# Optimization experiments

Hardware: AMD Instinct MI355X
Metric: run time of the kernel (lower is better)

The kernel has to match this reference:

```python
import jax, jax.numpy as jnp
import numpy as np

DIM = 192
NH = 4
B, H, W = 4, 128, 128


def _conv1x1(x, w, b):
    # x: [b,c,h,w], w: [o,c], b: [o]
    return jnp.einsum('oc,bchw->bohw', w, x) + b[None, :, None, None]


def _dwconv3(x, w, b):
    # depthwise 3x3, w: [C,1,3,3]
    y = jax.lax.conv_general_dilated(
        x, w, window_strides=(1, 1), padding='SAME',
        feature_group_count=x.shape[1],
        dimension_numbers=('NCHW', 'OIHW', 'NCHW'))
    return y + b[None, :, None, None]


def _to_heads(x, nh):
    b, c, h, w = x.shape
    return x.reshape(b, nh, c // nh, h * w)  # b head c (hw)


def _l2norm(x):
    # torch F.normalize(dim=-1): x / max(||x||, eps)
    n = jnp.sqrt(jnp.sum(x * x, axis=-1, keepdims=True))
    return x / jnp.maximum(n, 1e-12)


def _chan_attn(q, k, v, temp):
    # q,k,v: [b,head,c,n]; temp: [head,1,1] -> broadcasts over [b,head,c,c]
    scores = jnp.einsum('bhcn,bhdn->bhcd', q, k) * temp
    a = jax.nn.softmax(scores, axis=-1)
    return jnp.einsum('bhcd,bhdn->bhcn', a, v)


def setup_inputs() -> dict:
    key = jax.random.key(0)
    ks = jax.random.split(key, 16)
    d3 = 3 * DIM
    inp = {
        'sar': jax.random.normal(ks[0], (B, DIM, H, W), jnp.float32),
        'ms': jax.random.normal(ks[1], (B, DIM, H, W), jnp.float32),
        'ms_qkv_w': jax.random.normal(ks[2], (d3, DIM), jnp.float32) * 0.02,
        'ms_qkv_b': jnp.zeros((d3,), jnp.float32),
        'ms_dw_w': jax.random.normal(ks[3], (d3, 1, 3, 3), jnp.float32) * 0.1,
        'ms_dw_b': jnp.zeros((d3,), jnp.float32),
        'ms_temp': jnp.ones((NH, 1, 1), jnp.float32),
        'sar_qkv_w': jax.random.normal(ks[4], (d3, DIM), jnp.float32) * 0.02,
        'sar_qkv_b': jnp.zeros((d3,), jnp.float32),
        'sar_dw_w': jax.random.normal(ks[5], (d3, 1, 3, 3), jnp.float32) * 0.1,
        'sar_dw_b': jnp.zeros((d3,), jnp.float32),
        'sar_temp': jnp.ones((NH, 1, 1), jnp.float32),
        'ms_proj_w': jax.random.normal(ks[6], (DIM, 2 * DIM), jnp.float32) * 0.02,
        'ms_proj_b': jnp.zeros((DIM,), jnp.float32),
        'sar_proj_w': jax.random.normal(ks[7], (DIM, DIM), jnp.float32) * 0.02,
        'sar_proj_b': jnp.zeros((DIM,), jnp.float32),
    }
    return inp


def reference(sar, ms, ms_qkv_w, ms_qkv_b, ms_dw_w, ms_dw_b, ms_temp,
              sar_qkv_w, sar_qkv_b, sar_dw_w, sar_dw_b, sar_temp,
              ms_proj_w, ms_proj_b, sar_proj_w, sar_proj_b):
    b, c, h, w = ms.shape

    ms_qkv = _dwconv3(_conv1x1(ms, ms_qkv_w, ms_qkv_b), ms_dw_w, ms_dw_b)
    ms_q, ms_k, ms_v = jnp.split(ms_qkv, 3, axis=1)
    ms_q = _l2norm(_to_heads(ms_q, NH))
    ms_k = _l2norm(_to_heads(ms_k, NH))
    ms_v = _to_heads(ms_v, NH)

    sar_qkv = _dwconv3(_conv1x1(sar, sar_qkv_w, sar_qkv_b), sar_dw_w, sar_dw_b)
    sar_q, sar_k, sar_v = jnp.split(sar_qkv, 3, axis=1)
    sar_q = _l2norm(_to_heads(sar_q, NH))
    sar_k = _l2norm(_to_heads(sar_k, NH))
    sar_v = _to_heads(sar_v, NH)

    ms_self = _chan_attn(ms_q, ms_k, ms_v, ms_temp).reshape(b, c, h, w)
    sar_self = _chan_attn(sar_q, sar_k, sar_v, sar_temp).reshape(b, c, h, w)
    cross = _chan_attn(sar_q, ms_k, sar_v, ms_temp).reshape(b, c, h, w)

    sar_out = sar + _conv1x1(sar_self, sar_proj_w, sar_proj_b)
    ms_cat = jnp.concatenate([ms_self, cross + ms_self], axis=1)
    ms_out = ms + _conv1x1(ms_cat, ms_proj_w, ms_proj_b)
    return (sar_out, ms_out)
```

## Files before the change

### kernel.cpp

```cpp
#include <hip/hip_runtime.h>
#include <hip/hip_bf16.h>
#include <cstdint>

#define DIMC 192
#define BB 4
#define NN 16384
#define D3 576
#define CHD 48
#define WWID 128
#define HHGT 128
#define NCK 64
#define CKW 256

typedef short short8 __attribute__((ext_vector_type(8)));
typedef float f32x4 __attribute__((ext_vector_type(4)));

union FragU { uint4 u4; short8 s8; };

__device__ __forceinline__ float bf2f(uint16_t v) {
    return __uint_as_float(((uint32_t)v) << 16);
}
__device__ __forceinline__ float2 upk2(uint32_t u) {
    float2 r;
    r.x = __uint_as_float(u << 16);
    r.y = __uint_as_float(u & 0xffff0000u);
    return r;
}
__device__ __forceinline__ uint16_t f2bf(float f) {
    uint32_t x = __float_as_uint(f);
    return (uint16_t)((x + 0x7fffu + ((x >> 16) & 1u)) >> 16);
}
__device__ __forceinline__ uint4 pack8(const uint16_t* v) {
    uint4 u;
    u.x = (uint32_t)v[0] | ((uint32_t)v[1] << 16);
    u.y = (uint32_t)v[2] | ((uint32_t)v[3] << 16);
    u.z = (uint32_t)v[4] | ((uint32_t)v[5] << 16);
    u.w = (uint32_t)v[6] | ((uint32_t)v[7] << 16);
    return u;
}

__global__ __launch_bounds__(256) void k_prep(
    const float* __restrict__ w0, const float* __restrict__ w1,
    const float* __restrict__ w2, const float* __restrict__ w3,
    uint16_t* __restrict__ o0, uint16_t* __restrict__ o1,
    uint16_t* __restrict__ o2a, uint16_t* __restrict__ o2b,
    uint16_t* __restrict__ o3)
{
    int i = blockIdx.x * 256 + threadIdx.x;
    if (i < 110592) { o0[i] = f2bf(w0[i]); return; }
    i -= 110592;
    if (i < 110592) { o1[i] = f2bf(w1[i]); return; }
    i -= 110592;
    if (i < 36864) {
        const int o = i / DIMC, c = i % DIMC;
        o2a[i] = f2bf(w2[o * 384 + c] + w2[o * 384 + DIMC + c]);
        o2b[i] = f2bf(w2[o * 384 + DIMC + c]);
        return;
    }
    i -= 36864;
    if (i < 36864) o3[i] = f2bf(w3[i]);
}

__global__ __launch_bounds__(256, 2) void k_conv_both(
    const float* __restrict__ ms, const float* __restrict__ sarp,
    const uint16_t* __restrict__ w_ms, const uint16_t* __restrict__ w_sar,
    const float* __restrict__ b_ms, const float* __restrict__ b_sar,
    uint16_t* __restrict__ out_ms, uint16_t* __restrict__ out_sar)
{
    __shared__ uint16_t xs[128][200];
    __shared__ uint16_t wstA[64][200];
    const int t = threadIdx.x;
    const int bid = blockIdx.x;
    const int path = bid >> 9;
    const int rem = bid & 511;
    const int nb = rem & 127, b = rem >> 7;
    const int n0 = nb * 128;

    const float* x        = path ? sarp  : ms;
    const uint16_t* wsrc  = path ? w_sar : w_ms;
    const float* bias     = path ? b_sar : b_ms;
    uint16_t* out         = path ? out_sar : out_ms;

    const int lane = t & 63, wvid = t >> 6;
    const int lm = lane & 15, g = lane >> 4;
    const int wm = wvid >> 1, wn = wvid & 1;
    const int wm_ = t >> 2, wq = t & 3;

    {
        const int sn = t & 127, kh = t >> 7;
        const float* xcol = x + ((size_t)b * DIMC + kh * 96) * NN + n0 + sn;
        for (int u = 0; u < 12; ++u) {
            uint16_t vals[8];
#pragma unroll
            for (int j = 0; j < 8; ++j)
                vals[j] = f2bf(xcol[(size_t)(u * 8 + j) * NN]);
            *(uint4*)&xs[sn][(kh * 12 + u) * 8] = pack8(vals);
        }
    }
    {
        const uint16_t* wrow = wsrc + (size_t)wm_ * DIMC;
#pragma unroll
        for (int i = 0; i < 6; ++i) {
            const int unit = i * 4 + wq;
            *(uint4*)&wstA[wm_][unit * 8] = *(const uint4*)&wrow[unit * 8];
        }
    }
    __syncthreads();

    FragU bfr[6][4];
#pragma unroll
    for (int ks = 0; ks < 6; ++ks)
#pragma unroll
        for (int nj = 0; nj < 4; ++nj) {
            const int row = wn * 64 + nj * 16 + lm;
            bfr[ks][nj].u4 = *(const uint4*)&xs[row][ks * 32 + g * 8];
        }
    __syncthreads();

    uint16_t* xsf  = &xs[0][0];
    uint16_t* wstB = xsf;
    uint16_t* sw   = xsf + 12800 + wvid * 2304;

    for (int mb = 0; mb < 9; ++mb) {
        const uint16_t* cur = (mb & 1) ? wstB : &wstA[0][0];
        uint16_t* nxt       = (mb & 1) ? &wstA[0][0] : wstB;
        uint4 wreg[6];
        if (mb < 8) {
            const uint16_t* wrow = wsrc + (size_t)((mb + 1) * 64 + wm_) * DIMC;
#pragma unroll
            for (int i = 0; i < 6; ++i)
                wreg[i] = *(const uint4*)&wrow[(i * 4 + wq) * 8];
        }
        f32x4 acc[2][4];
#pragma unroll
        for (int mi = 0; mi < 2; ++mi)
#pragma unroll
            for (int nj = 0; nj < 4; ++nj) acc[mi][nj] = (f32x4){0.f, 0.f, 0.f, 0.f};
#pragma unroll
        for (int ks = 0; ks < 6; ++ks) {
            FragU afr[2];
#pragma unroll
            for (int mi = 0; mi < 2; ++mi) {
                const int row = wm * 32 + mi * 16 + lm;
                afr[mi].u4 = *(const uint4*)&cur[row * 200 + ks * 32 + g * 8];
            }
#pragma unroll
            for (int mi = 0; mi < 2; ++mi)
#pragma unroll
                for (int nj = 0; nj < 4; ++nj)
                    acc[mi][nj] = __builtin_amdgcn_mfma_f32_16x16x32_bf16(
                        afr[mi].s8, bfr[ks][nj].s8, acc[mi][nj], 0, 0, 0);
        }
        if (mb < 8) {
#pragma unroll
            for (int i = 0; i < 6; ++i)
                *(uint4*)&nxt[wm_ * 200 + (i * 4 + wq) * 8] = wreg[i];
        }
#pragma unroll
        for (int mi = 0; mi < 2; ++mi) {
            const int rbase = mb * 64 + wm * 32 + mi * 16 + g * 4;
            const float4 bv = *(const float4*)&bias[rbase];
            const float bva[4] = {bv.x, bv.y, bv.z, bv.w};
#pragma unroll
            for (int nj = 0; nj < 4; ++nj)
#pragma unroll
                for (int r = 0; r < 4; ++r)
                    sw[(mi * 16 + g * 4 + r) * 72 + nj * 16 + lm] =
                        f2bf(acc[mi][nj][r] + bva[r]);
        }
        const int l8 = lane & 7, r8 = lane >> 3;
#pragma unroll
        for (int pass = 0; pass < 4; ++pass) {
            const int rr = pass * 8 + r8;
            uint4 v = *(const uint4*)&sw[rr * 72 + l8 * 8];
            const int grow = mb * 64 + wm * 32 + rr;
            *(uint4*)&out[((size_t)b * D3 + grow) * NN + n0 + wn * 64 + l8 * 8] = v;
        }
        __syncthreads();
    }
}

__global__ __launch_bounds__(256, 2) void k_proj_both(
    const uint16_t* __restrict__ sar_self, const uint16_t* __restrict__ ms_self,
    const uint16_t* __restrict__ crossb,
    const uint16_t* __restrict__ wp_sar, const uint16_t* __restrict__ wp1_ms,
    const uint16_t* __restrict__ wp2_ms,
    const float* __restrict__ b_sar, const float* __restrict__ b_ms,
    const float* __restrict__ resid_sar, const float* __restrict__ resid_ms,
    float* __restrict__ out_sar, float* __restrict__ out_ms)
{
    __shared__ uint16_t xs[128][200];
    __shared__ uint16_t wstA[64][200];
    const int t = threadIdx.x;
    const int bid = blockIdx.x;
    const int path = bid >> 9;
    const int rem = bid & 511;
    const int nb = rem & 127, b = rem >> 7;
    const int n0 = nb * 128;
    const int nph = path ? 2 : 1;

    const float* bias  = path ? b_ms : b_sar;
    const float* resid = path ? resid_ms : resid_sar;
    float* out         = path ? out_ms : out_sar;

    const int lane = t & 63, wvid = t >> 6;
    const int lm = lane & 15, g = lane >> 4;
    const int wm = wvid >> 1, wn = wvid & 1;
    const int wm_ = t >> 2, wq = t & 3;

    uint16_t* xsf  = &xs[0][0];
    uint16_t* wstB = xsf;

    f32x4 acc[3][2][4];
#pragma unroll
    for (int mb = 0; mb < 3; ++mb)
#pragma unroll
        for (int mi = 0; mi < 2; ++mi)
#pragma unroll
            for (int nj = 0; nj < 4; ++nj) acc[mb][mi][nj] = (f32x4){0.f, 0.f, 0.f, 0.f};

    for (int ph = 0; ph < nph; ++ph) {
        const uint16_t* xsrc = path ? (ph ? crossb : ms_self) : sar_self;
        const uint16_t* wsrc = path ? (ph ? wp2_ms : wp1_ms) : wp_sar;
        {
            const int p = t & 63, kg = t >> 6;
            const uint16_t* xcol = xsrc + ((size_t)b * DIMC + kg * 48) * NN + n0 + p * 2;
            for (int chn = 0; chn < 6; ++chn) {
                uint32_t v[8];
#pragma unroll
                for (int j = 0; j < 8; ++j)
                    v[j] = *(const uint32_t*)&xcol[(size_t)(chn * 8 + j) * NN];
                uint4 lo4, hi4;
                lo4.x = (v[0] & 0xffffu) | (v[1] << 16);
                lo4.y = (v[2] & 0xffffu) | (v[3] << 16);
                lo4.z = (v[4] & 0xffffu) | (v[5] << 16);
                lo4.w = (v[6] & 0xffffu) | (v[7] << 16);
                hi4.x = (v[0] >> 16) | (v[1] & 0xffff0000u);
                hi4.y = (v[2] >> 16) | (v[3] & 0xffff0000u);
                hi4.z = (v[4] >> 16) | (v[5] & 0xffff0000u);
                hi4.w = (v[6] >> 16) | (v[7] & 0xffff0000u);
                *(uint4*)&xs[p * 2][(kg * 6 + chn) * 8]     = lo4;
                *(uint4*)&xs[p * 2 + 1][(kg * 6 + chn) * 8] = hi4;
            }
        }
        {
            const uint16_t* wrow = wsrc + (size_t)wm_ * DIMC;
#pragma unroll
            for (int i = 0; i < 6; ++i) {
                const int unit = i * 4 + wq;
                *(uint4*)&wstA[wm_][unit * 8] = *(const uint4*)&wrow[unit * 8];
            }
        }
        __syncthreads();
        FragU bfr[6][4];
#pragma unroll
        for (int ks = 0; ks < 6; ++ks)
#pragma unroll
            for (int nj = 0; nj < 4; ++nj) {
                const int row = wn * 64 + nj * 16 + lm;
                bfr[ks][nj].u4 = *(const uint4*)&xs[row][ks * 32 + g * 8];
            }
        __syncthreads();

        for (int mb = 0; mb < 3; ++mb) {
            const uint16_t* cur = (mb & 1) ? wstB : &wstA[0][0];
            uint16_t* nxt       = (mb & 1) ? &wstA[0][0] : wstB;
            uint4 wreg[6];
            if (mb < 2) {
                const uint16_t* wrow = wsrc + (size_t)((mb + 1) * 64 + wm_) * DIMC;
#pragma unroll
                for (int i = 0; i < 6; ++i)
                    wreg[i] = *(const uint4*)&wrow[(i * 4 + wq) * 8];
            }
#pragma unroll
            for (int ks = 0; ks < 6; ++ks) {
                FragU afr[2];
#pragma unroll
                for (int mi = 0; mi < 2; ++mi) {
                    const int row = wm * 32 + mi * 16 + lm;
                    afr[mi].u4 = *(const uint4*)&cur[row * 200 + ks * 32 + g * 8];
                }
#pragma unroll
                for (int mi = 0; mi < 2; ++mi)
#pragma unroll
                    for (int nj = 0; nj < 4; ++nj)
                        acc[mb][mi][nj] = __builtin_amdgcn_mfma_f32_16x16x32_bf16(
                            afr[mi].s8, bfr[ks][nj].s8, acc[mb][mi][nj], 0, 0, 0);
            }
            if (mb < 2) {
#pragma unroll
                for (int i = 0; i < 6; ++i)
                    *(uint4*)&nxt[wm_ * 200 + (i * 4 + wq) * 8] = wreg[i];
            }
            __syncthreads();
        }
    }
#pragma unroll
    for (int mb = 0; mb < 3; ++mb)
#pragma unroll
        for (int mi = 0; mi < 2; ++mi) {
            const int rbase = mb * 64 + wm * 32 + mi * 16 + g * 4;
            const float4 bv = *(const float4*)&bias[rbase];
            const float bva[4] = {bv.x, bv.y, bv.z, bv.w};
#pragma unroll
            for (int nj = 0; nj < 4; ++nj) {
                const int gcol = n0 + wn * 64 + nj * 16 + lm;
#pragma unroll
                for (int r = 0; r < 4; ++r) {
                    const size_t idx = ((size_t)b * DIMC + rbase + r) * NN + gcol;
                    out[idx] = resid[idx] + acc[mb][mi][nj][r] + bva[r];
                }
            }
        }
}

__global__ __launch_bounds__(256) void k_dw_both(
    const uint16_t* __restrict__ in0, const uint16_t* __restrict__ in1,
    const float* __restrict__ w_ms, const float* __restrict__ w_sar,
    const float* __restrict__ b_ms, const float* __restrict__ b_sar,
    uint16_t* __restrict__ out0, uint16_t* __restrict__ out1)
{
    __shared__ uint16_t lds[34 * 136];
    const int t = threadIdx.x;
    const int bid = blockIdx.x;
    const int yb = bid & 3;
    int bc = bid >> 2;
    const int path = (bc >= BB * D3);
    if (path) bc -= BB * D3;
    const int ch = bc % D3;
    const uint16_t* in = path ? in1 : in0;
    const float* w9    = path ? w_sar : w_ms;
    const float* bias  = path ? b_sar : b_ms;
    uint16_t* out      = path ? out1 : out0;

    const int y0 = yb * 32;
    const uint16_t* p = in + (size_t)bc * NN;

#pragma unroll
    for (int it = 0; it < 3; ++it) {
        const int u = it * 256 + t;
        if (u < 34 * 16) {
            const int r = u >> 4, seg = u & 15;
            const int gy = y0 - 1 + r;
            uint4 v = (gy >= 0 && gy < HHGT)
                ? *(const uint4*)(p + gy * WWID + seg * 8)
                : (uint4){0u, 0u, 0u, 0u};
            *(uint4*)&lds[r * 136 + seg * 8] = v;
        }
    }
    float wv[9];
#pragma unroll
    for (int k = 0; k < 9; ++k) wv[k] = w9[ch * 9 + k];
    const float base = bias[ch];
    __syncthreads();

    const int lr = t >> 3;
    const int x0 = (t & 7) * 16;
    float rv[3][18];
#pragma unroll
    for (int dy = 0; dy < 3; ++dy) {
        const uint16_t* lp = &lds[(lr + dy) * 136 + x0];
        uint4 a = *(const uint4*)lp;
        uint4 bq = *(const uint4*)(lp + 8);
        const uint16_t* av = (const uint16_t*)&a;
        const uint16_t* bv2 = (const uint16_t*)&bq;
#pragma unroll
        for (int j = 0; j < 8; ++j) {
            rv[dy][1 + j] = bf2f(av[j]);
            rv[dy][9 + j] = bf2f(bv2[j]);
        }
        rv[dy][0]  = (x0 > 0) ? bf2f(lds[(lr + dy) * 136 + x0 - 1]) : 0.f;
        rv[dy][17] = (x0 + 16 < WWID) ? bf2f(lds[(lr + dy) * 136 + x0 + 16]) : 0.f;
    }
    uint16_t ov[16];
#pragma unroll
    for (int j = 0; j < 16; ++j) {
        float a = base;
#pragma unroll
        for (int dy = 0; dy < 3; ++dy)
            a = fmaf(rv[dy][j], wv[dy * 3],
                fmaf(rv[dy][j + 1], wv[dy * 3 + 1],
                fmaf(rv[dy][j + 2], wv[dy * 3 + 2], a)));
        ov[j] = f2bf(a);
    }
    uint16_t* ob = out + (size_t)bc * NN + (y0 + lr) * WWID + x0;
    *(uint4*)ob       = pack8(&ov[0]);
    *(uint4*)(ob + 8) = pack8(&ov[8]);
}

__global__ __launch_bounds__(256) void k_scores_mfma(
    const uint16_t* __restrict__ qkv_ms, const uint16_t* __restrict__ qkv_sar,
    float* __restrict__ partial, float* __restrict__ sumsq)
{
    const int t = threadIdx.x;
    const int bid = blockIdx.x;
    const int ck = bid & (NCK - 1);
    const int pid = bid / NCK;
    const int h = pid & 3, b = pid >> 2;
    const int n0 = ck * CKW;
    const int lane = t & 63, w = t >> 6;

    const uint16_t* qm  = qkv_ms  + ((size_t)b * D3 + h * CHD) * NN;
    const uint16_t* km  = qkv_ms  + ((size_t)b * D3 + DIMC + h * CHD) * NN;
    const uint16_t* qsr = qkv_sar + ((size_t)b * D3 + h * CHD) * NN;
    const uint16_t* ksr = qkv_sar + ((size_t)b * D3 + DIMC + h * CHD) * NN;

    if (w < 3) {
        const uint16_t* qb = (w == 0) ? qm : qsr;
        const uint16_t* kb = (w == 1) ? ksr : km;
        const int lm = lane & 15, g = lane >> 4;
        f32x4 acc[3][3];
#pragma unroll
        for (int i = 0; i < 3; ++i)
#pragma unroll
            for (int j = 0; j < 3; ++j) acc[i][j] = (f32x4){0.f, 0.f, 0.f, 0.f};
#pragma unroll 2
        for (int kk = 0; kk < CKW / 32; ++kk) {
            const int nb2 = n0 + kk * 32 + g * 8;
            FragU qf[3], kf[3];
#pragma unroll
            for (int i = 0; i < 3; ++i)
                qf[i].u4 = *(const uint4*)&qb[(size_t)(i * 16 + lm) * NN + nb2];
#pragma unroll
            for (int j = 0; j < 3; ++j)
                kf[j].u4 = *(const uint4*)&kb[(size_t)(j * 16 + lm) * NN + nb2];
#pragma unroll
            for (int i = 0; i < 3; ++i)
#pragma unroll
                for (int j = 0; j < 3; ++j)
                    acc[i][j] = __builtin_amdgcn_mfma_f32_16x16x32_bf16(
                        qf[i].s8, kf[j].s8, acc[i][j], 0, 0, 0);
        }
        float* pd = partial + (((size_t)pid * 3 + w) * NCK + ck) * 2304;
        const int g4 = g * 4;
#pragma unroll
        for (int i = 0; i < 3; ++i)
#pragma unroll
            for (int j = 0; j < 3; ++j)
#pragma unroll
                for (int r = 0; r < 4; ++r)
                    pd[(i * 16 + g4 + r) * 48 + j * 16 + lm] = acc[i][j][r];
    } else {
#pragma unroll
        for (int rep = 0; rep < 3; ++rep) {
            const int rid = rep * 64 + lane;
            const int s = rid / CHD, c = rid % CHD;
            const uint16_t* rowp =
                (s == 0) ? qm  + (size_t)c * NN :
                (s == 1) ? km  + (size_t)c * NN :
                (s == 2) ? qsr + (size_t)c * NN :
                           ksr + (size_t)c * NN;
            float sum = 0.f;
#pragma unroll 4
            for (int u = 0; u < CKW / 8; ++u) {
                uint4 v = *(const uint4*)&rowp[n0 + u * 8];
                uint32_t uu[4] = {v.x, v.y, v.z, v.w};
#pragma unroll
                for (int q = 0; q < 4; ++q) {
                    float2 f = upk2(uu[q]);
                    sum = fmaf(f.x, f.x, fmaf(f.y, f.y, sum));
                }
            }
            sumsq[(((size_t)pid * NCK + ck) * 4 + s) * CHD + c] = sum;
        }
    }
}

__global__ __launch_bounds__(64) void k_softmax(
    const float* __restrict__ partial, const float* __restrict__ sumsq,
    const float* __restrict__ ms_temp, const float* __restrict__ sar_temp,
    float* __restrict__ A)
{
    const int lane = threadIdx.x;
    const int bi = blockIdx.x;
    const int c = bi % 48;
    const int pid = bi / 48;
    const int h = pid & 3, b = (pid >> 2) & 3, type = pid >> 4;
    const int pid16 = b * 4 + h;
    float s;
    if (lane < 48) {
        float accv = 0.f;
        const float* pp = partial + ((size_t)pid16 * 3 + type) * NCK * 2304 + c * 48 + lane;
#pragma unroll 8
        for (int ck = 0; ck < NCK; ++ck) accv += pp[(size_t)ck * 2304];
        const int qset = (type == 0) ? 0 : 2;
        const int kset = (type == 1) ? 3 : 1;
        float qsum = 0.f, ksum = 0.f;
        const float* sq = sumsq + (size_t)pid16 * NCK * 4 * CHD;
#pragma unroll 8
        for (int ck = 0; ck < NCK; ++ck) {
            qsum += sq[ck * 4 * CHD + qset * CHD + c];
            ksum += sq[ck * 4 * CHD + kset * CHD + lane];
        }
        const float tval = (type == 1) ? sar_temp[h] : ms_temp[h];
        const float qsc = 1.0f / fmaxf(sqrtf(qsum), 1e-12f);
        const float ksc = 1.0f / fmaxf(sqrtf(ksum), 1e-12f);
        s = accv * qsc * ksc * tval;
    } else {
        s = -3.0e38f;
    }
    float m = s;
#pragma unroll
    for (int o = 32; o > 0; o >>= 1) m = fmaxf(m, __shfl_xor(m, o));
    float e = (lane < 48) ? __expf(s - m) : 0.f;
    float sum = e;
#pragma unroll
    for (int o = 32; o > 0; o >>= 1) sum += __shfl_xor(sum, o);
    if (lane < 48) A[(size_t)pid * 2304 + c * 48 + lane] = e / sum;
}

__global__ __launch_bounds__(256) void k_apply_mfma(
    const float* __restrict__ A, const uint16_t* __restrict__ qkv_ms,
    const uint16_t* __restrict__ qkv_sar, uint16_t* __restrict__ attn)
{
    __shared__ uint16_t vs[256][40];
    __shared__ uint16_t as[48][40];
    __shared__ uint16_t sw_all[4][48][72];
    const int t = threadIdx.x;
    const int nb = blockIdx.x & 63;
    const int pid = blockIdx.x >> 6;
    const int h = pid & 3, b = (pid >> 2) & 3, type = pid >> 4;
    const int n0 = nb * 256;
    const uint16_t* vsrc = (type == 0) ? qkv_ms : qkv_sar;
    const uint16_t* vb = vsrc + ((size_t)b * D3 + 2 * DIMC + (size_t)h * CHD) * NN;
    const float* Ap = A + (size_t)pid * 2304;

    const int lane = t & 63, wvid = t >> 6;
    const int lm = lane & 15, g = lane >> 4;

    f32x4 acc[3][4];
#pragma unroll
    for (int i = 0; i < 3; ++i)
#pragma unroll
        for (int j = 0; j < 4; ++j) acc[i][j] = (f32x4){0.f, 0.f, 0.f, 0.f};

    for (int k0 = 0; k0 < 64; k0 += 32) {
        __syncthreads();
#pragma unroll
        for (int kh = 0; kh < 2; ++kh) {
            uint16_t vals[16];
#pragma unroll
            for (int j = 0; j < 16; ++j) {
                const int d = k0 + kh * 16 + j;
                vals[j] = (d < CHD) ? vb[(size_t)d * NN + n0 + t] : (uint16_t)0;
            }
            const int u0 = (2 * kh) ^ ((t >> 3) & 3);
            const int u1 = (2 * kh + 1) ^ ((t >> 3) & 3);
            *(uint4*)&vs[t][u0 * 8] = pack8(&vals[0]);
            *(uint4*)&vs[t][u1 * 8] = pack8(&vals[8]);
        }
        if (t < 192) {
            const int c = t >> 2, dq = t & 3;
            uint16_t av[8];
#pragma unroll
            for (int i = 0; i < 8; ++i) {
                const int d = k0 + dq * 8 + i;
                av[i] = (d < CHD) ? f2bf(Ap[c * CHD + d]) : (uint16_t)0;
            }
            const int u = dq ^ ((c >> 3) & 3);
            *(uint4*)&as[c][u * 8] = pack8(av);
        }
        __syncthreads();
        FragU afr[3], bfr[4];
#pragma unroll
        for (int mi = 0; mi < 3; ++mi) {
            const int row = mi * 16 + lm;
            afr[mi].u4 = *(const uint4*)&as[row][(g ^ ((row >> 3) & 3)) * 8];
        }
#pragma unroll
        for (int nj = 0; nj < 4; ++nj) {
            const int row = wvid * 64 + nj * 16 + lm;
            bfr[nj].u4 = *(const uint4*)&vs[row][(g ^ ((row >> 3) & 3)) * 8];
        }
#pragma unroll
        for (int mi = 0; mi < 3; ++mi)
#pragma unroll
            for (int nj = 0; nj < 4; ++nj)
                acc[mi][nj] = __builtin_amdgcn_mfma_f32_16x16x32_bf16(
                    afr[mi].s8, bfr[nj].s8, acc[mi][nj], 0, 0, 0);
    }

    uint16_t* ob = attn + (size_t)type * BB * DIMC * NN +
                   ((size_t)b * DIMC + (size_t)h * CHD) * NN;
    uint16_t* sw = &sw_all[wvid][0][0];
#pragma unroll
    for (int mi = 0; mi < 3; ++mi)
#pragma unroll
        for (int nj = 0; nj < 4; ++nj)
#pragma unroll
            for (int r = 0; r < 4; ++r)
                sw[(mi * 16 + g * 4 + r) * 72 + nj * 16 + lm] = f2bf(acc[mi][nj][r]);
    const int l8 = lane & 7, r8 = lane >> 3;
#pragma unroll
    for (int pass = 0; pass < 6; ++pass) {
        const int rr = pass * 8 + r8;
        uint4 v = *(const uint4*)&sw[rr * 72 + l8 * 8];
        *(uint4*)&ob[(size_t)rr * NN + n0 + wvid * 64 + l8 * 8] = v;
    }
}

extern "C" void kernel_launch(void* const* d_in, const int* in_sizes, int n_in,
                              void* d_out, int out_size, void* d_ws, size_t ws_size,
                              hipStream_t stream)
{
    const float* sar        = (const float*)d_in[0];
    const float* ms         = (const float*)d_in[1];
    const float* ms_qkv_w   = (const float*)d_in[2];
    const float* ms_qkv_b   = (const float*)d_in[3];
    const float* ms_dw_w    = (const float*)d_in[4];
    const float* ms_dw_b    = (const float*)d_in[5];
    const float* ms_temp    = (const float*)d_in[6];
    const float* sar_qkv_w  = (const float*)d_in[7];
    const float* sar_qkv_b  = (const float*)d_in[8];
    const float* sar_dw_w   = (const float*)d_in[9];
    const float* sar_dw_b   = (const float*)d_in[10];
    const float* sar_temp   = (const float*)d_in[11];
    const float* ms_proj_w  = (const float*)d_in[12];
    const float* ms_proj_b  = (const float*)d_in[13];
    const float* sar_proj_w = (const float*)d_in[14];
    const float* sar_proj_b = (const float*)d_in[15];

    char* ws = (char*)d_ws;
    uint16_t* tmp     = (uint16_t*)(ws);
    uint16_t* tmp2    = (uint16_t*)(d_out);
    uint16_t* qkv_ms  = (uint16_t*)(ws + 75497472ull);
    uint16_t* qkv_sar = (uint16_t*)(ws + 150994944ull);
    float* partial    = (float*)(ws);
    float* sumsq      = (float*)(ws + 33554432ull);
    float* Amat       = (float*)(ws + 230043648ull);
    uint16_t* wq_ms   = (uint16_t*)(ws + 230486016ull);
    uint16_t* wq_sar  = (uint16_t*)(ws + 230707200ull);
    uint16_t* wp1_ms  = (uint16_t*)(ws + 230928384ull);
    uint16_t* wp2_ms  = (uint16_t*)(ws + 231002112ull);
    uint16_t* wp_sar  = (uint16_t*)(ws + 231075840ull);
    uint16_t* attn    = tmp;

    float* out_sar = (float*)d_out;
    float* out_ms  = out_sar + (size_t)BB * DIMC * NN;

    dim3 b256(256);
    k_prep<<<dim3(1152), b256, 0, stream>>>(ms_qkv_w, sar_qkv_w, ms_proj_w, sar_proj_w,
                                            wq_ms, wq_sar, wp1_ms, wp2_ms, wp_sar);
    k_conv_both<<<dim3(1024), b256, 0, stream>>>(
        ms, sar, wq_ms, wq_sar, ms_qkv_b, sar_qkv_b, tmp, tmp2);
    k_dw_both<<<dim3(2 * BB * D3 * 4), b256, 0, stream>>>(
        tmp, tmp2, ms_dw_w, sar_dw_w, ms_dw_b, sar_dw_b, qkv_ms, qkv_sar);

    k_scores_mfma<<<dim3(16 * NCK), b256, 0, stream>>>(qkv_ms, qkv_sar, partial, sumsq);
    k_softmax<<<dim3(48 * 48), dim3(64), 0, stream>>>(partial, sumsq, ms_temp, sar_temp, Amat);
    k_apply_mfma<<<dim3(48 * 64), b256, 0, stream>>>(Amat, qkv_ms, qkv_sar, attn);

    uint16_t* ms_self  = attn;
    uint16_t* sar_self = attn + (size_t)BB * DIMC * NN;
    uint16_t* crossb   = attn + 2ull * BB * DIMC * NN;
    k_proj_both<<<dim3(1024), b256, 0, stream>>>(
        sar_self, ms_self, crossb, wp_sar, wp1_ms, wp2_ms,
        sar_proj_b, ms_proj_b, sar, ms, out_sar, out_ms);
}
```

Before: 282.6 us.

## Load GEMM weight fragments directly from global and shrink LDS for occupancy

In the conv and projection kernels, the weight tile is no longer staged and double-buffered through shared memory. Each wave now loads its MFMA A fragments straight from global memory, which L2 should cache. This removes the wstA buffer and the per-iteration barriers, cutting LDS use so launch bounds can rise to 3 blocks per CU. An XOR swizzle is also added to the activation tile to reduce LDS bank conflicts, at the cost of more global load latency inside the MFMA loop.

```diff
diff --git a/kernel.cpp b/kernel.cpp
--- a/kernel.cpp
+++ b/kernel.cpp
@@ -61,14 +61,13 @@
     if (i < 36864) o3[i] = f2bf(w3[i]);
 }
 
-__global__ __launch_bounds__(256, 2) void k_conv_both(
+__global__ __launch_bounds__(256, 3) void k_conv_both(
     const float* __restrict__ ms, const float* __restrict__ sarp,
     const uint16_t* __restrict__ w_ms, const uint16_t* __restrict__ w_sar,
     const float* __restrict__ b_ms, const float* __restrict__ b_sar,
     uint16_t* __restrict__ out_ms, uint16_t* __restrict__ out_sar)
 {
     __shared__ uint16_t xs[128][200];
-    __shared__ uint16_t wstA[64][200];
     const int t = threadIdx.x;
     const int bid = blockIdx.x;
     const int path = bid >> 9;
@@ -84,25 +83,17 @@
     const int lane = t & 63, wvid = t >> 6;
     const int lm = lane & 15, g = lane >> 4;
     const int wm = wvid >> 1, wn = wvid & 1;
-    const int wm_ = t >> 2, wq = t & 3;
 
     {
         const int sn = t & 127, kh = t >> 7;
+        const int sg = (sn >> 3) & 3;
         const float* xcol = x + ((size_t)b * DIMC + kh * 96) * NN + n0 + sn;
         for (int u = 0; u < 12; ++u) {
             uint16_t vals[8];
 #pragma unroll
             for (int j = 0; j < 8; ++j)
                 vals[j] = f2bf(xcol[(size_t)(u * 8 + j) * NN]);
-            *(uint4*)&xs[sn][(kh * 12 + u) * 8] = pack8(vals);
-        }
-    }
-    {
-        const uint16_t* wrow = wsrc + (size_t)wm_ * DIMC;
-#pragma unroll
-        for (int i = 0; i < 6; ++i) {
-            const int unit = i * 4 + wq;
-            *(uint4*)&wstA[wm_][unit * 8] = *(const uint4*)&wrow[unit * 8];
+            *(uint4*)&xs[sn][((kh * 12 + u) ^ sg) * 8] = pack8(vals);
         }
     }
     __syncthreads();
@@ -113,24 +104,13 @@
 #pragma unroll
         for (int nj = 0; nj < 4; ++nj) {
             const int row = wn * 64 + nj * 16 + lm;
-            bfr[ks][nj].u4 = *(const uint4*)&xs[row][ks * 32 + g * 8];
+            bfr[ks][nj].u4 = *(const uint4*)&xs[row][((ks * 4 + g) ^ ((row >> 3) & 3)) * 8];
         }
     __syncthreads();
 
-    uint16_t* xsf  = &xs[0][0];
-    uint16_t* wstB = xsf;
-    uint16_t* sw   = xsf + 12800 + wvid * 2304;
+    uint16_t* sw = &xs[0][0] + wvid * 2304;
 
     for (int mb = 0; mb < 9; ++mb) {
-        const uint16_t* cur = (mb & 1) ? wstB : &wstA[0][0];
-        uint16_t* nxt       = (mb & 1) ? &wstA[0][0] : wstB;
-        uint4 wreg[6];
-        if (mb < 8) {
-            const uint16_t* wrow = wsrc + (size_t)((mb + 1) * 64 + wm_) * DIMC;
-#pragma unroll
-            for (int i = 0; i < 6; ++i)
-                wreg[i] = *(const uint4*)&wrow[(i * 4 + wq) * 8];
-        }
         f32x4 acc[2][4];
 #pragma unroll
         for (int mi = 0; mi < 2; ++mi)
@@ -141,8 +121,8 @@
             FragU afr[2];
 #pragma unroll
             for (int mi = 0; mi < 2; ++mi) {
-                const int row = wm * 32 + mi * 16 + lm;
-                afr[mi].u4 = *(const uint4*)&cur[row * 200 + ks * 32 + g * 8];
+                const int m = mb * 64 + wm * 32 + mi * 16 + lm;
+                afr[mi].u4 = *(const uint4*)&wsrc[(size_t)m * DIMC + ks * 32 + g * 8];
             }
 #pragma unroll
             for (int mi = 0; mi < 2; ++mi)
@@ -150,11 +130,6 @@
                 for (int nj = 0; nj < 4; ++nj)
                     acc[mi][nj] = __builtin_amdgcn_mfma_f32_16x16x32_bf16(
                         afr[mi].s8, bfr[ks][nj].s8, acc[mi][nj], 0, 0, 0);
-        }
-        if (mb < 8) {
-#pragma unroll
-            for (int i = 0; i < 6; ++i)
-                *(uint4*)&nxt[wm_ * 200 + (i * 4 + wq) * 8] = wreg[i];
         }
 #pragma unroll
         for (int mi = 0; mi < 2; ++mi) {
@@ -176,11 +151,10 @@
             const int grow = mb * 64 + wm * 32 + rr;
             *(uint4*)&out[((size_t)b * D3 + grow) * NN + n0 + wn * 64 + l8 * 8] = v;
         }
-        __syncthreads();
-    }
-}
-
-__global__ __launch_bounds__(256, 2) void k_proj_both(
+    }
+}
+
+__global__ __launch_bounds__(256, 3) void k_proj_both(
     const uint16_t* __restrict__ sar_self, const uint16_t* __restrict__ ms_self,
     const uint16_t* __restrict__ crossb,
     const uint16_t* __restrict__ wp_sar, const uint16_t* __restrict__ wp1_ms,
@@ -190,7 +164,6 @@
     float* __restrict__ out_sar, float* __restrict__ out_ms)
 {
     __shared__ uint16_t xs[128][200];
-    __shared__ uint16_t wstA[64][200];
     const int t = threadIdx.x;
     const int bid = blockIdx.x;
     const int path = bid >> 9;
@@ -206,10 +179,6 @@
     const int lane = t & 63, wvid = t >> 6;
     const int lm = lane & 15, g = lane >> 4;
     const int wm = wvid >> 1, wn = wvid & 1;
-    const int wm_ = t >> 2, wq = t & 3;
-
-    uint16_t* xsf  = &xs[0][0];
-    uint16_t* wstB = xsf;
 
     f32x4 acc[3][2][4];
 #pragma unroll
@@ -224,6 +193,7 @@
         const uint16_t* wsrc = path ? (ph ? wp2_ms : wp1_ms) : wp_sar;
         {
             const int p = t & 63, kg = t >> 6;
+            const int sg = (p >> 2) & 3;
             const uint16_t* xcol = xsrc + ((size_t)b * DIMC + kg * 48) * NN + n0 + p * 2;
             for (int chn = 0; chn < 6; ++chn) {
                 uint32_t v[8];
@@ -239,16 +209,9 @@
                 hi4.y = (v[2] >> 16) | (v[3] & 0xffff0000u);
                 hi4.z = (v[4] >> 16) | (v[5] & 0xffff0000u);
                 hi4.w = (v[6] >> 16) | (v[7] & 0xffff0000u);
-                *(uint4*)&xs[p * 2][(kg * 6 + chn) * 8]     = lo4;
-                *(uint4*)&xs[p * 2 + 1][(kg * 6 + chn) * 8] = hi4;
-            }
-        }
-        {
-            const uint16_t* wrow = wsrc + (size_t)wm_ * DIMC;
-#pragma unroll
-            for (int i = 0; i < 6; ++i) {
-                const int unit = i * 4 + wq;
-                *(uint4*)&wstA[wm_][unit * 8] = *(const uint4*)&wrow[unit * 8];
+                const int unit = (kg * 6 + chn) ^ sg;
+                *(uint4*)&xs[p * 2][unit * 8]     = lo4;
+                *(uint4*)&xs[p * 2 + 1][unit * 8] = hi4;
             }
         }
         __syncthreads();
@@ -258,27 +221,18 @@
 #pragma unroll
             for (int nj = 0; nj < 4; ++nj) {
                 const int row = wn * 64 + nj * 16 + lm;
-                bfr[ks][nj].u4 = *(const uint4*)&xs[row][ks * 32 + g * 8];
+                bfr[ks][nj].u4 = *(const uint4*)&xs[row][((ks * 4 + g) ^ ((row >> 3) & 3)) * 8];
             }
         __syncthreads();
 
         for (int mb = 0; mb < 3; ++mb) {
-            const uint16_t* cur = (mb & 1) ? wstB : &wstA[0][0];
-            uint16_t* nxt       = (mb & 1) ? &wstA[0][0] : wstB;
-            uint4 wreg[6];
-            if (mb < 2) {
-                const uint16_t* wrow = wsrc + (size_t)((mb + 1) * 64 + wm_) * DIMC;
-#pragma unroll
-                for (int i = 0; i < 6; ++i)
-                    wreg[i] = *(const uint4*)&wrow[(i * 4 + wq) * 8];
-            }
 #pragma unroll
             for (int ks = 0; ks < 6; ++ks) {
                 FragU afr[2];
 #pragma unroll
                 for (int mi = 0; mi < 2; ++mi) {
-                    const int row = wm * 32 + mi * 16 + lm;
-                    afr[mi].u4 = *(const uint4*)&cur[row * 200 + ks * 32 + g * 8];
+                    const int m = mb * 64 + wm * 32 + mi * 16 + lm;
+                    afr[mi].u4 = *(const uint4*)&wsrc[(size_t)m * DIMC + ks * 32 + g * 8];
                 }
 #pragma unroll
                 for (int mi = 0; mi < 2; ++mi)
@@ -287,12 +241,6 @@
                         acc[mb][mi][nj] = __builtin_amdgcn_mfma_f32_16x16x32_bf16(
                             afr[mi].s8, bfr[ks][nj].s8, acc[mb][mi][nj], 0, 0, 0);
             }
-            if (mb < 2) {
-#pragma unroll
-                for (int i = 0; i < 6; ++i)
-                    *(uint4*)&nxt[wm_ * 200 + (i * 4 + wq) * 8] = wreg[i];
-            }
-            __syncthreads();
         }
     }
 #pragma unroll
```

New measurement: 421.3 us. +49.1%, slower.

## Use 512-thread blocks and XOR-swizzled LDS in conv and projection GEMMs

Applied to the files above, without the earlier changes.

Both 1x1 conv GEMM kernels go from 256 to 512 threads per block, with 8 waves each covering a 32x32 tile instead of 4 waves covering 32x64. Per-thread load, accumulator and fragment arrays are halved, which lowers register pressure and adds more waves to hide global-memory latency. LDS reads and writes for activations and weights now use XOR-swizzled chunk indices to cut bank conflicts. The cost is more address arithmetic, more barrier participants and a higher occupancy request in launch bounds, which may cause register spills.

```diff
diff --git a/kernel.cpp b/kernel.cpp
--- a/kernel.cpp
+++ b/kernel.cpp
@@ -61,7 +61,7 @@
     if (i < 36864) o3[i] = f2bf(w3[i]);
 }
 
-__global__ __launch_bounds__(256, 2) void k_conv_both(
+__global__ __launch_bounds__(512, 4) void k_conv_both(
     const float* __restrict__ ms, const float* __restrict__ sarp,
     const uint16_t* __restrict__ w_ms, const uint16_t* __restrict__ w_sar,
     const float* __restrict__ b_ms, const float* __restrict__ b_sar,
@@ -83,78 +83,81 @@
 
     const int lane = t & 63, wvid = t >> 6;
     const int lm = lane & 15, g = lane >> 4;
-    const int wm = wvid >> 1, wn = wvid & 1;
-    const int wm_ = t >> 2, wq = t & 3;
+    const int wm = wvid >> 2, wn = wvid & 3;
+    const int wm_ = t >> 3, wq = t & 7;
 
     {
-        const int sn = t & 127, kh = t >> 7;
-        const float* xcol = x + ((size_t)b * DIMC + kh * 96) * NN + n0 + sn;
-        for (int u = 0; u < 12; ++u) {
+        const int sn = t & 127, kq = t >> 7;
+        const int sg = (sn >> 3) & 3;
+        const float* xcol = x + ((size_t)b * DIMC + kq * 48) * NN + n0 + sn;
+        for (int u = 0; u < 6; ++u) {
             uint16_t vals[8];
 #pragma unroll
             for (int j = 0; j < 8; ++j)
                 vals[j] = f2bf(xcol[(size_t)(u * 8 + j) * NN]);
-            *(uint4*)&xs[sn][(kh * 12 + u) * 8] = pack8(vals);
+            *(uint4*)&xs[sn][((kq * 6 + u) ^ sg) * 8] = pack8(vals);
         }
     }
     {
         const uint16_t* wrow = wsrc + (size_t)wm_ * DIMC;
 #pragma unroll
-        for (int i = 0; i < 6; ++i) {
-            const int unit = i * 4 + wq;
-            *(uint4*)&wstA[wm_][unit * 8] = *(const uint4*)&wrow[unit * 8];
+        for (int i = 0; i < 3; ++i) {
+            const int unit = i * 8 + wq;
+            *(uint4*)&wstA[wm_][(unit ^ (wm_ & 7)) * 8] = *(const uint4*)&wrow[unit * 8];
         }
     }
     __syncthreads();
 
-    FragU bfr[6][4];
+    FragU bfr[6][2];
 #pragma unroll
     for (int ks = 0; ks < 6; ++ks)
 #pragma unroll
-        for (int nj = 0; nj < 4; ++nj) {
-            const int row = wn * 64 + nj * 16 + lm;
-            bfr[ks][nj].u4 = *(const uint4*)&xs[row][ks * 32 + g * 8];
+        for (int nj = 0; nj < 2; ++nj) {
+            const int row = wn * 32 + nj * 16 + lm;
+            bfr[ks][nj].u4 = *(const uint4*)&xs[row][((ks * 4 + g) ^ ((row >> 3) & 3)) * 8];
         }
     __syncthreads();
 
     uint16_t* xsf  = &xs[0][0];
     uint16_t* wstB = xsf;
-    uint16_t* sw   = xsf + 12800 + wvid * 2304;
+    uint16_t* sw   = xsf + 12800 + wvid * 1280;
 
     for (int mb = 0; mb < 9; ++mb) {
         const uint16_t* cur = (mb & 1) ? wstB : &wstA[0][0];
         uint16_t* nxt       = (mb & 1) ? &wstA[0][0] : wstB;
-        uint4 wreg[6];
+        uint4 wreg[3];
         if (mb < 8) {
             const uint16_t* wrow = wsrc + (size_t)((mb + 1) * 64 + wm_) * DIMC;
 #pragma unroll
-            for (int i = 0; i < 6; ++i)
-                wreg[i] = *(const uint4*)&wrow[(i * 4 + wq) * 8];
-        }
-        f32x4 acc[2][4];
+            for (int i = 0; i < 3; ++i)
+                wreg[i] = *(const uint4*)&wrow[(i * 8 + wq) * 8];
+        }
+        f32x4 acc[2][2];
 #pragma unroll
         for (int mi = 0; mi < 2; ++mi)
 #pragma unroll
-            for (int nj = 0; nj < 4; ++nj) acc[mi][nj] = (f32x4){0.f, 0.f, 0.f, 0.f};
+            for (int nj = 0; nj < 2; ++nj) acc[mi][nj] = (f32x4){0.f, 0.f, 0.f, 0.f};
 #pragma unroll
         for (int ks = 0; ks < 6; ++ks) {
             FragU afr[2];
 #pragma unroll
             for (int mi = 0; mi < 2; ++mi) {
                 const int row = wm * 32 + mi * 16 + lm;
-                afr[mi].u4 = *(const uint4*)&cur[row * 200 + ks * 32 + g * 8];
+                afr[mi].u4 = *(const uint4*)&cur[row * 200 + ((ks * 4 + g) ^ (row & 7)) * 8];
             }
 #pragma unroll
             for (int mi = 0; mi < 2; ++mi)
 #pragma unroll
-                for (int nj = 0; nj < 4; ++nj)
+                for (int nj = 0; nj < 2; ++nj)
                     acc[mi][nj] = __builtin_amdgcn_mfma_f32_16x16x32_bf16(
                         afr[mi].s8, bfr[ks][nj].s8, acc[mi][nj], 0, 0, 0);
         }
         if (mb < 8) {
 #pragma unroll
-            for (int i = 0; i < 6; ++i)
-                *(uint4*)&nxt[wm_ * 200 + (i * 4 + wq) * 8] = wreg[i];
+            for (int i = 0; i < 3; ++i) {
+                const int unit = i * 8 + wq;
+                *(uint4*)&nxt[wm_ * 200 + ((unit ^ (wm_ & 7))) * 8] = wreg[i];
+            }
         }
 #pragma unroll
         for (int mi = 0; mi < 2; ++mi) {
@@ -162,25 +165,26 @@
             const float4 bv = *(const float4*)&bias[rbase];
             const float bva[4] = {bv.x, bv.y, bv.z, bv.w};
 #pragma unroll
-            for (int nj = 0; nj < 4; ++nj)
+            for (int nj = 0; nj < 2; ++nj)
 #pragma unroll
                 for (int r = 0; r < 4; ++r)
-                    sw[(mi * 16 + g * 4 + r) * 72 + nj * 16 + lm] =
+                    sw[(mi * 16 + g * 4 + r) * 40 + nj * 16 + lm] =
                         f2bf(acc[mi][nj][r] + bva[r]);
         }
-        const int l8 = lane & 7, r8 = lane >> 3;
-#pragma unroll
-        for (int pass = 0; pass < 4; ++pass) {
-            const int rr = pass * 8 + r8;
-            uint4 v = *(const uint4*)&sw[rr * 72 + l8 * 8];
-            const int grow = mb * 64 + wm * 32 + rr;
-            *(uint4*)&out[((size_t)b * D3 + grow) * NN + n0 + wn * 64 + l8 * 8] = v;
+        {
+            const int row2 = lane >> 1, q = lane & 1;
+            uint4 v0 = *(const uint4*)&sw[row2 * 40 + q * 16];
+            uint4 v1 = *(const uint4*)&sw[row2 * 40 + q * 16 + 8];
+            const int grow = mb * 64 + wm * 32 + row2;
+            uint16_t* ob = &out[((size_t)b * D3 + grow) * NN + n0 + wn * 32 + q * 16];
+            *(uint4*)ob       = v0;
+            *(uint4*)(ob + 8) = v1;
         }
         __syncthreads();
     }
 }
 
-__global__ __launch_bounds__(256, 2) void k_proj_both(
+__global__ __launch_bounds__(512, 4) void k_proj_both(
     const uint16_t* __restrict__ sar_self, const uint16_t* __restrict__ ms_self,
     const uint16_t* __restrict__ crossb,
     const uint16_t* __restrict__ wp_sar, const uint16_t* __restrict__ wp1_ms,
@@ -205,27 +209,28 @@
 
     const int lane = t & 63, wvid = t >> 6;
     const int lm = lane & 15, g = lane >> 4;
-    const int wm = wvid >> 1, wn = wvid & 1;
-    const int wm_ = t >> 2, wq = t & 3;
+    const int wm = wvid >> 2, wn = wvid & 3;
+    const int wm_ = t >> 3, wq = t & 7;
 
     uint16_t* xsf  = &xs[0][0];
     uint16_t* wstB = xsf;
 
-    f32x4 acc[3][2][4];
+    f32x4 acc[3][2][2];
 #pragma unroll
     for (int mb = 0; mb < 3; ++mb)
 #pragma unroll
         for (int mi = 0; mi < 2; ++mi)
 #pragma unroll
-            for (int nj = 0; nj < 4; ++nj) acc[mb][mi][nj] = (f32x4){0.f, 0.f, 0.f, 0.f};
+            for (int nj = 0; nj < 2; ++nj) acc[mb][mi][nj] = (f32x4){0.f, 0.f, 0.f, 0.f};
 
     for (int ph = 0; ph < nph; ++ph) {
         const uint16_t* xsrc = path ? (ph ? crossb : ms_self) : sar_self;
         const uint16_t* wsrc = path ? (ph ? wp2_ms : wp1_ms) : wp_sar;
         {
             const int p = t & 63, kg = t >> 6;
-            const uint16_t* xcol = xsrc + ((size_t)b * DIMC + kg * 48) * NN + n0 + p * 2;
-            for (int chn = 0; chn < 6; ++chn) {
+            const int sg = (p >> 2) & 3;
+            const uint16_t* xcol = xsrc + ((size_t)b * DIMC + kg * 24) * NN + n0 + p * 2;
+            for (int chn = 0; chn < 3; ++chn) {
                 uint32_t v[8];
 #pragma unroll
                 for (int j = 0; j < 8; ++j)
@@ -239,38 +244,39 @@
                 hi4.y = (v[2] >> 16) | (v[3] & 0xffff0000u);
                 hi4.z = (v[4] >> 16) | (v[5] & 0xffff0000u);
                 hi4.w = (v[6] >> 16) | (v[7] & 0xffff0000u);
-                *(uint4*)&xs[p * 2][(kg * 6 + chn) * 8]     = lo4;
-                *(uint4*)&xs[p * 2 + 1][(kg * 6 + chn) * 8] = hi4;
+                const int unit = (kg * 3 + chn) ^ sg;
+                *(uint4*)&xs[p * 2][unit * 8]     = lo4;
+                *(uint4*)&xs[p * 2 + 1][unit * 8] = hi4;
             }
         }
         {
             const uint16_t* wrow = wsrc + (size_t)wm_ * DIMC;
 #pragma unroll
-            for (int i = 0; i < 6; ++i) {
-                const int unit = i * 4 + wq;
-                *(uint4*)&wstA[wm_][unit * 8] = *(const uint4*)&wrow[unit * 8];
+            for (int i = 0; i < 3; ++i) {
+                const int unit = i * 8 + wq;
+                *(uint4*)&wstA[wm_][(unit ^ (wm_ & 7)) * 8] = *(const uint4*)&wrow[unit * 8];
             }
         }
         __syncthreads();
-        FragU bfr[6][4];
+        FragU bfr[6][2];
 #pragma unroll
         for (int ks = 0; ks < 6; ++ks)
 #pragma unroll
-            for (int nj = 0; nj < 4; ++nj) {
-                const int row = wn * 64 + nj * 16 + lm;
-                bfr[ks][nj].u4 = *(const uint4*)&xs[row][ks * 32 + g * 8];
+            for (int nj = 0; nj < 2; ++nj) {
+                const int row = wn * 32 + nj * 16 + lm;
+                bfr[ks][nj].u4 = *(const uint4*)&xs[row][((ks * 4 + g) ^ ((row >> 3) & 3)) * 8];
             }
         __syncthreads();
 
         for (int mb = 0; mb < 3; ++mb) {
             const uint16_t* cur = (mb & 1) ? wstB : &wstA[0][0];
             uint16_t* nxt       = (mb & 1) ? &wstA[0][0] : wstB;
-            uint4 wreg[6];
+            uint4 wreg[3];
             if (mb < 2) {
                 const uint16_t* wrow = wsrc + (size_t)((mb + 1) * 64 + wm_) * DIMC;
 #pragma unroll
-                for (int i = 0; i < 6; ++i)
-                    wreg[i] = *(const uint4*)&wrow[(i * 4 + wq) * 8];
+                for (int i = 0; i < 3; ++i)
+                    wreg[i] = *(const uint4*)&wrow[(i * 8 + wq) * 8];
             }
 #pragma unroll
             for (int ks = 0; ks < 6; ++ks) {
@@ -278,19 +284,21 @@
 #pragma unroll
                 for (int mi = 0; mi < 2; ++mi) {
                     const int row = wm * 32 + mi * 16 + lm;
-                    afr[mi].u4 = *(const uint4*)&cur[row * 200 + ks * 32 + g * 8];
+                    afr[mi].u4 = *(const uint4*)&cur[row * 200 + ((ks * 4 + g) ^ (row & 7)) * 8];
                 }
 #pragma unroll
                 for (int mi = 0; mi < 2; ++mi)
 #pragma unroll
-                    for (int nj = 0; nj < 4; ++nj)
+                    for (int nj = 0; nj < 2; ++nj)
                         acc[mb][mi][nj] = __builtin_amdgcn_mfma_f32_16x16x32_bf16(
                             afr[mi].s8, bfr[ks][nj].s8, acc[mb][mi][nj], 0, 0, 0);
             }
             if (mb < 2) {
 #pragma unroll
-                for (int i = 0; i < 6; ++i)
-                    *(uint4*)&nxt[wm_ * 200 + (i * 4 + wq) * 8] = wreg[i];
+                for (int i = 0; i < 3; ++i) {
+                    const int unit = i * 8 + wq;
+                    *(uint4*)&nxt[wm_ * 200 + ((unit ^ (wm_ & 7))) * 8] = wreg[i];
+                }
             }
             __syncthreads();
         }
@@ -303,8 +311,8 @@
             const float4 bv = *(const float4*)&bias[rbase];
             const float bva[4] = {bv.x, bv.y, bv.z, bv.w};
 #pragma unroll
-            for (int nj = 0; nj < 4; ++nj) {
-                const int gcol = n0 + wn * 64 + nj * 16 + lm;
+            for (int nj = 0; nj < 2; ++nj) {
+                const int gcol = n0 + wn * 32 + nj * 16 + lm;
 #pragma unroll
                 for (int r = 0; r < 4; ++r) {
                     const size_t idx = ((size_t)b * DIMC + rbase + r) * NN + gcol;
@@ -641,7 +649,7 @@
     dim3 b256(256);
     k_prep<<<dim3(1152), b256, 0, stream>>>(ms_qkv_w, sar_qkv_w, ms_proj_w, sar_proj_w,
                                             wq_ms, wq_sar, wp1_ms, wp2_ms, wp_sar);
-    k_conv_both<<<dim3(1024), b256, 0, stream>>>(
+    k_conv_both<<<dim3(1024), dim3(512), 0, stream>>>(
         ms, sar, wq_ms, wq_sar, ms_qkv_b, sar_qkv_b, tmp, tmp2);
     k_dw_both<<<dim3(2 * BB * D3 * 4), b256, 0, stream>>>(
         tmp, tmp2, ms_dw_w, sar_dw_w, ms_dw_b, sar_dw_b, qkv_ms, qkv_sar);
@@ -653,7 +661,7 @@
     uint16_t* ms_self  = attn;
     uint16_t* sar_self = attn + (size_t)BB * DIMC * NN;
     uint16_t* crossb   = attn + 2ull * BB * DIMC * NN;
-    k_proj_both<<<dim3(1024), b256, 0, stream>>>(
+    k_proj_both<<<dim3(1024), dim3(512), 0, stream>>>(
         sar_self, ms_self, crossb, wp_sar, wp1_ms, wp2_ms,
         sar_proj_b, ms_proj_b, sar, ms, out_sar, out_ms);
 }
```

After: 324.4 us. 1.15x slower.

## Drop separate weight LDS buffer in conv/proj kernels to fit three blocks per CU

Applied to the files above, without the earlier changes.

Removes the dedicated 64x200 weight staging array from both GEMM kernels. Weight tiles are now staged in the reused xs region after the activation fragments have been loaded into registers. The conv kernel goes from double buffering to a single weight buffer with an extra barrier per step. Launch bounds are raised to three blocks per CU to take advantage of the smaller LDS footprint. The cost is tighter register budgets, which may cause spills, and less overlap between weight loads and MFMA work.

```diff
diff --git a/kernel.cpp b/kernel.cpp
--- a/kernel.cpp
+++ b/kernel.cpp
@@ -61,14 +61,13 @@
     if (i < 36864) o3[i] = f2bf(w3[i]);
 }
 
-__global__ __launch_bounds__(256, 2) void k_conv_both(
+__global__ __launch_bounds__(256, 3) void k_conv_both(
     const float* __restrict__ ms, const float* __restrict__ sarp,
     const uint16_t* __restrict__ w_ms, const uint16_t* __restrict__ w_sar,
     const float* __restrict__ b_ms, const float* __restrict__ b_sar,
     uint16_t* __restrict__ out_ms, uint16_t* __restrict__ out_sar)
 {
     __shared__ uint16_t xs[128][200];
-    __shared__ uint16_t wstA[64][200];
     const int t = threadIdx.x;
     const int bid = blockIdx.x;
     const int path = bid >> 9;
@@ -86,6 +85,13 @@
     const int wm = wvid >> 1, wn = wvid & 1;
     const int wm_ = t >> 2, wq = t & 3;
 
+    uint4 wreg[6];
+    {
+        const uint16_t* wrow = wsrc + (size_t)wm_ * DIMC;
+#pragma unroll
+        for (int i = 0; i < 6; ++i)
+            wreg[i] = *(const uint4*)&wrow[(i * 4 + wq) * 8];
+    }
     {
         const int sn = t & 127, kh = t >> 7;
         const float* xcol = x + ((size_t)b * DIMC + kh * 96) * NN + n0 + sn;
@@ -97,14 +103,6 @@
             *(uint4*)&xs[sn][(kh * 12 + u) * 8] = pack8(vals);
         }
     }
-    {
-        const uint16_t* wrow = wsrc + (size_t)wm_ * DIMC;
-#pragma unroll
-        for (int i = 0; i < 6; ++i) {
-            const int unit = i * 4 + wq;
-            *(uint4*)&wstA[wm_][unit * 8] = *(const uint4*)&wrow[unit * 8];
-        }
-    }
     __syncthreads();
 
     FragU bfr[6][4];
@@ -117,14 +115,16 @@
         }
     __syncthreads();
 
-    uint16_t* xsf  = &xs[0][0];
-    uint16_t* wstB = xsf;
-    uint16_t* sw   = xsf + 12800 + wvid * 2304;
+    uint16_t* xsf = &xs[0][0];
+    uint16_t* wst = xsf;
+    uint16_t* sw  = xsf + 12800 + wvid * 2304;
+
+#pragma unroll
+    for (int i = 0; i < 6; ++i)
+        *(uint4*)&wst[wm_ * 200 + (i * 4 + wq) * 8] = wreg[i];
+    __syncthreads();
 
     for (int mb = 0; mb < 9; ++mb) {
-        const uint16_t* cur = (mb & 1) ? wstB : &wstA[0][0];
-        uint16_t* nxt       = (mb & 1) ? &wstA[0][0] : wstB;
-        uint4 wreg[6];
         if (mb < 8) {
             const uint16_t* wrow = wsrc + (size_t)((mb + 1) * 64 + wm_) * DIMC;
 #pragma unroll
@@ -142,7 +142,7 @@
 #pragma unroll
             for (int mi = 0; mi < 2; ++mi) {
                 const int row = wm * 32 + mi * 16 + lm;
-                afr[mi].u4 = *(const uint4*)&cur[row * 200 + ks * 32 + g * 8];
+                afr[mi].u4 = *(const uint4*)&wst[row * 200 + ks * 32 + g * 8];
             }
 #pragma unroll
             for (int mi = 0; mi < 2; ++mi)
@@ -150,11 +150,6 @@
                 for (int nj = 0; nj < 4; ++nj)
                     acc[mi][nj] = __builtin_amdgcn_mfma_f32_16x16x32_bf16(
                         afr[mi].s8, bfr[ks][nj].s8, acc[mi][nj], 0, 0, 0);
-        }
-        if (mb < 8) {
-#pragma unroll
-            for (int i = 0; i < 6; ++i)
-                *(uint4*)&nxt[wm_ * 200 + (i * 4 + wq) * 8] = wreg[i];
         }
 #pragma unroll
         for (int mi = 0; mi < 2; ++mi) {
@@ -177,10 +172,16 @@
             *(uint4*)&out[((size_t)b * D3 + grow) * NN + n0 + wn * 64 + l8 * 8] = v;
         }
         __syncthreads();
-    }
-}
-
-__global__ __launch_bounds__(256, 2) void k_proj_both(
+        if (mb < 8) {
+#pragma unroll
+            for (int i = 0; i < 6; ++i)
+                *(uint4*)&wst[wm_ * 200 + (i * 4 + wq) * 8] = wreg[i];
+            __syncthreads();
+        }
+    }
+}
+
+__global__ __launch_bounds__(256, 3) void k_proj_both(
     const uint16_t* __restrict__ sar_self, const uint16_t* __restrict__ ms_self,
     const uint16_t* __restrict__ crossb,
     const uint16_t* __restrict__ wp_sar, const uint16_t* __restrict__ wp1_ms,
@@ -190,7 +191,6 @@
     float* __restrict__ out_sar, float* __restrict__ out_ms)
 {
     __shared__ uint16_t xs[128][200];
-    __shared__ uint16_t wstA[64][200];
     const int t = threadIdx.x;
     const int bid = blockIdx.x;
     const int path = bid >> 9;
@@ -208,8 +208,9 @@
     const int wm = wvid >> 1, wn = wvid & 1;
     const int wm_ = t >> 2, wq = t & 3;
 
-    uint16_t* xsf  = &xs[0][0];
-    uint16_t* wstB = xsf;
+    uint16_t* xsf = &xs[0][0];
+    uint16_t* wbA = xsf;
+    uint16_t* wbB = xsf + 12800;
 
     f32x4 acc[3][2][4];
 #pragma unroll
@@ -222,6 +223,13 @@
     for (int ph = 0; ph < nph; ++ph) {
         const uint16_t* xsrc = path ? (ph ? crossb : ms_self) : sar_self;
         const uint16_t* wsrc = path ? (ph ? wp2_ms : wp1_ms) : wp_sar;
+        uint4 wreg[6];
+        {
+            const uint16_t* wrow = wsrc + (size_t)wm_ * DIMC;
+#pragma unroll
+            for (int i = 0; i < 6; ++i)
+                wreg[i] = *(const uint4*)&wrow[(i * 4 + wq) * 8];
+        }
         {
             const int p = t & 63, kg = t >> 6;
             const uint16_t* xcol = xsrc + ((size_t)b * DIMC + kg * 48) * NN + n0 + p * 2;
@@ -243,14 +251,6 @@
                 *(uint4*)&xs[p * 2 + 1][(kg * 6 + chn) * 8] = hi4;
             }
         }
-        {
-            const uint16_t* wrow = wsrc + (size_t)wm_ * DIMC;
-#pragma unroll
-            for (int i = 0; i < 6; ++i) {
-                const int unit = i * 4 + wq;
-                *(uint4*)&wstA[wm_][unit * 8] = *(const uint4*)&wrow[unit * 8];
-            }
-        }
         __syncthreads();
         FragU bfr[6][4];
 #pragma unroll
@@ -261,11 +261,14 @@
                 bfr[ks][nj].u4 = *(const uint4*)&xs[row][ks * 32 + g * 8];
             }
         __syncthreads();
+#pragma unroll
+        for (int i = 0; i < 6; ++i)
+            *(uint4*)&wbA[wm_ * 200 + (i * 4 + wq) * 8] = wreg[i];
+        __syncthreads();
 
         for (int mb = 0; mb < 3; ++mb) {
-            const uint16_t* cur = (mb & 1) ? wstB : &wstA[0][0];
-            uint16_t* nxt       = (mb & 1) ? &wstA[0][0] : wstB;
-            uint4 wreg[6];
+            const uint16_t* cur = (mb & 1) ? wbB : wbA;
+            uint16_t* nxt       = (mb & 1) ? wbA : wbB;
             if (mb < 2) {
                 const uint16_t* wrow = wsrc + (size_t)((mb + 1) * 64 + wm_) * DIMC;
 #pragma unroll
```

Result: slower. 521.4 us (+84.5%).
